# Performance work log

Hardware: AMD Instinct MI355X
Metric: run time of the kernel (lower is better)

## Reference

```python
import jax, jax.numpy as jnp
import numpy as np


def setup_inputs() -> dict:
    key = jax.random.key(0)
    ks = jax.random.split(key, 6)
    B, H, Tq, Tk, D, HID = 2, 4, 512, 512, 64, 128
    return {
        "q": jax.random.normal(ks[0], (B, H, Tq, D), dtype=jnp.float32),
        "k": jax.random.normal(ks[1], (B, H, Tk, D), dtype=jnp.float32),
        # W1 stored math-layout [Dq+Dk, hidden] (torch Linear weight is its transpose)
        "W1": jax.random.normal(ks[2], (2 * D, HID), dtype=jnp.float32) * (1.0 / np.sqrt(2 * D)),
        "b1": jax.random.normal(ks[3], (HID,), dtype=jnp.float32) * 0.02,
        "W2": jax.random.normal(ks[4], (HID, 1), dtype=jnp.float32) * (1.0 / np.sqrt(HID)),
        "b2": jax.random.normal(ks[5], (1,), dtype=jnp.float32) * 0.02,
    }


def reference(q, k, W1, b1, W2, b2):
    """Pairwise MLP scores s[b,h,i,j] = W2 . relu(W1 @ [q_i; k_j] + b1) + b2.

    Linear over cat(q,k) decomposes into separate q/k projections that are
    broadcast-summed, avoiding the [B,H,Tq,Tk,Dq+Dk] concat tensor (same math).
    """
    Dq = q.shape[-1]
    qh = jnp.einsum("bhqd,dc->bhqc", q, W1[:Dq])   # [B,H,Tq,hid]
    kh = jnp.einsum("bhkd,dc->bhkc", k, W1[Dq:])   # [B,H,Tk,hid]
    h = jax.nn.relu(qh[:, :, :, None, :] + kh[:, :, None, :, :] + b1)  # [B,H,Tq,Tk,hid]
    s = jnp.einsum("bhqkc,c->bhqk", h, W2[:, 0]) + b2[0]
    return s
```

## Files before the change

kernel.cpp:

```cpp
#include <hip/hip_runtime.h>

#define T    512
#define D    64
#define HID  128
#define NBH  8
#define NP   (HID / 2)

typedef _Float16 h2 __attribute__((ext_vector_type(2)));

static __device__ __forceinline__ h2 bc_h2(float f) {
    return __builtin_bit_cast(h2, f);
}

__global__ __launch_bounds__(256, 2) void proj_kernel(
    const float* __restrict__ q, const float* __restrict__ k,
    const float* __restrict__ W1, const float* __restrict__ b1,
    h2* __restrict__ qh_h, h2* __restrict__ kh_h)
{
    const int bid    = blockIdx.x;
    const int bh     = bid >> 6;
    const int src    = (bid >> 5) & 1;
    const int chunk  = (bid >> 2) & 7;
    const int csplit = bid & 3;
    const int base_c = csplit * 32;

    const float* __restrict__ X = (src == 0) ? q : k;
    h2* __restrict__ outp       = (src == 0) ? qh_h : kh_h;

    __shared__ float w1t[32][68];

    const int tid = threadIdx.x;
    for (int idx = tid; idx < 32 * 64; idx += 256) {
        const int cc = idx & 31;
        const int d  = idx >> 5;
        w1t[cc][d] = W1[(src * D + d) * HID + base_c + cc];
    }
    __syncthreads();

    const int r  = tid & 63;
    const int cg = tid >> 6;
    const int i  = chunk * 64 + r;

    float xr[D];
    const float4* xrow = (const float4*)(X + (size_t)(bh * T + i) * D);
    #pragma unroll
    for (int t = 0; t < D / 4; ++t) {
        const float4 v = xrow[t];
        xr[4*t+0] = v.x; xr[4*t+1] = v.y; xr[4*t+2] = v.z; xr[4*t+3] = v.w;
    }

    #pragma unroll
    for (int pp = 0; pp < 4; ++pp) {
        const int cc0 = cg * 8 + 2 * pp;
        float acc0 = (src == 0) ? b1[base_c + cc0]     : 0.0f;
        float acc1 = (src == 0) ? b1[base_c + cc0 + 1] : 0.0f;
        const float4* w0 = (const float4*)(&w1t[cc0][0]);
        const float4* w1 = (const float4*)(&w1t[cc0 + 1][0]);
        #pragma unroll
        for (int t = 0; t < D / 4; ++t) {
            const float4 a = w0[t];
            const float4 b = w1[t];
            acc0 += xr[4*t+0]*a.x + xr[4*t+1]*a.y + xr[4*t+2]*a.z + xr[4*t+3]*a.w;
            acc1 += xr[4*t+0]*b.x + xr[4*t+1]*b.y + xr[4*t+2]*b.z + xr[4*t+3]*b.w;
        }
        h2 v;
        v.x = (_Float16)acc0;
        v.y = (_Float16)acc1;
        const int p = csplit * 16 + cg * 4 + pp;
        outp[(size_t)(bh * NP + p) * T + i] = v;
    }
}

__global__ __launch_bounds__(256, 2) void score_kernel(
    const h2* __restrict__ qh_h, const h2* __restrict__ kh_h,
    const float* __restrict__ W2, const float* __restrict__ b2,
    float* __restrict__ out)
{
    const int bid = blockIdx.x;
    const int bh  = bid >> 6;
    const int it  = (bid >> 3) & 7;
    const int jt  = bid & 7;
    const int i0  = it * 64;
    const int j0  = jt * 64;

    __shared__ h2 qt2[NP + 1][64];
    __shared__ h2 kt2[NP + 1][64];
    __shared__ h2 w2h[NP + 4];

    const int tid = threadIdx.x;
    for (int idx = tid; idx < 2 * NP * 16; idx += 256) {
        const int tile = idx >> 10;
        const int p    = (idx >> 4) & 63;
        const int g    = idx & 15;
        const h2* srcp = tile ? kh_h : qh_h;
        const int o0   = tile ? j0 : i0;
        float4 v = ((const float4*)(srcp + (size_t)(bh * NP + p) * T + o0))[g];
        if (tile) ((float4*)&kt2[p][0])[g] = v;
        else      ((float4*)&qt2[p][0])[g] = v;
    }
    if (tid < NP) {
        h2 w;
        w.x = (_Float16)W2[2 * tid];
        w.y = (_Float16)W2[2 * tid + 1];
        w2h[tid] = w;
    }
    __syncthreads();

    const int tx = tid & 15;
    const int ty = tid >> 4;

    const h2* __restrict__ qb = &qt2[0][4 * ty];
    const h2* __restrict__ kb = &kt2[0][4 * tx];

    float acc[4][4];
    #pragma unroll
    for (int m = 0; m < 4; ++m)
        #pragma unroll
        for (int n = 0; n < 4; ++n)
            acc[m][n] = 0.0f;

    const h2 hzero = (h2)(_Float16)0.0f;

    float4 qf = *(const float4*)qb;
    float4 kf = *(const float4*)kb;
    float4 w4 = *(const float4*)&w2h[0];

    for (int pg = 0; pg < 16; ++pg) {
        const float4 w4n = *(const float4*)&w2h[4 * pg + 4];
        #pragma unroll
        for (int s = 0; s < 4; ++s) {
            const int p = 4 * pg + s;
            const float4 qn = *(const float4*)(qb + (size_t)(p + 1) * 64);
            const float4 kn = *(const float4*)(kb + (size_t)(p + 1) * 64);

            const h2 w = bc_h2(s == 0 ? w4.x : s == 1 ? w4.y
                             : s == 2 ? w4.z : w4.w);
            const h2 qv[4] = {bc_h2(qf.x), bc_h2(qf.y), bc_h2(qf.z), bc_h2(qf.w)};
            const h2 kv[4] = {bc_h2(kf.x), bc_h2(kf.y), bc_h2(kf.z), bc_h2(kf.w)};
            #pragma unroll
            for (int m = 0; m < 4; ++m) {
                #pragma unroll
                for (int n = 0; n < 4; ++n) {
                    h2 u = qv[m] + kv[n];
                    u = __builtin_elementwise_max(u, hzero);
                    acc[m][n] = __builtin_amdgcn_fdot2(u, w, acc[m][n], false);
                }
            }
            qf = qn;
            kf = kn;
        }
        w4 = w4n;
    }

    const float bb = b2[0];
    #pragma unroll
    for (int m = 0; m < 4; ++m) {
        const int i = i0 + 4 * ty + m;
        float4 o;
        o.x = acc[m][0] + bb;
        o.y = acc[m][1] + bb;
        o.z = acc[m][2] + bb;
        o.w = acc[m][3] + bb;
        ((float4*)(out + (size_t)(bh * T + i) * T + j0))[tx] = o;
    }
}

extern "C" void kernel_launch(void* const* d_in, const int* in_sizes, int n_in,
                              void* d_out, int out_size, void* d_ws, size_t ws_size,
                              hipStream_t stream) {
    const float* q  = (const float*)d_in[0];
    const float* k  = (const float*)d_in[1];
    const float* W1 = (const float*)d_in[2];
    const float* b1 = (const float*)d_in[3];
    const float* W2 = (const float*)d_in[4];
    const float* b2 = (const float*)d_in[5];
    float* out = (float*)d_out;

    h2* qh_h = (h2*)d_ws;
    h2* kh_h = qh_h + (size_t)NBH * NP * T;

    proj_kernel<<<512, 256, 0, stream>>>(q, k, W1, b1, qh_h, kh_h);
    score_kernel<<<512, 256, 0, stream>>>(qh_h, kh_h, W2, b2, out);
}
```

Baseline: 91.35 us.

## Halve score tile width, double grid, and use inline-asm packed ReLU

The score kernel now uses 64x32 output tiles with a 4x2 micro-tile per thread, launching 1024 blocks instead of 512, with occupancy hint raised to 4 blocks per SM. The explicit register double-buffering of LDS loads is replaced by a simple unrolled loop. The ReLU is now an inline v_pk_max_f16 with an inline constant zero. The goal is more blocks for better CU coverage and latency hiding. The cost is less register reuse per thread, more LDS reads per FMA, and duplicated q-tile loads across blocks.

Result: no change. 92.85 us (+1.6%).

```diff
diff --git a/kernel.cpp b/kernel.cpp
--- a/kernel.cpp
+++ b/kernel.cpp
@@ -10,6 +10,12 @@
 
 static __device__ __forceinline__ h2 bc_h2(float f) {
     return __builtin_bit_cast(h2, f);
+}
+
+static __device__ __forceinline__ h2 relu_h2(h2 x) {
+    h2 r;
+    asm("v_pk_max_f16 %0, %1, 0" : "=v"(r) : "v"(x));
+    return r;
 }
 
 __global__ __launch_bounds__(256, 2) void proj_kernel(
@@ -71,32 +77,36 @@
     }
 }
 
-__global__ __launch_bounds__(256, 2) void score_kernel(
+__global__ __launch_bounds__(256, 4) void score_kernel(
     const h2* __restrict__ qh_h, const h2* __restrict__ kh_h,
     const float* __restrict__ W2, const float* __restrict__ b2,
     float* __restrict__ out)
 {
     const int bid = blockIdx.x;
-    const int bh  = bid >> 6;
-    const int it  = (bid >> 3) & 7;
-    const int jt  = bid & 7;
+    const int bh  = bid >> 7;
+    const int it  = (bid >> 4) & 7;
+    const int jt  = bid & 15;
     const int i0  = it * 64;
-    const int j0  = jt * 64;
+    const int j0  = jt * 32;
 
-    __shared__ h2 qt2[NP + 1][64];
-    __shared__ h2 kt2[NP + 1][64];
-    __shared__ h2 w2h[NP + 4];
+    __shared__ h2 qt2[NP][64];
+    __shared__ h2 kt2[NP][32];
+    __shared__ h2 w2h[NP];
 
     const int tid = threadIdx.x;
-    for (int idx = tid; idx < 2 * NP * 16; idx += 256) {
-        const int tile = idx >> 10;
-        const int p    = (idx >> 4) & 63;
-        const int g    = idx & 15;
-        const h2* srcp = tile ? kh_h : qh_h;
-        const int o0   = tile ? j0 : i0;
-        float4 v = ((const float4*)(srcp + (size_t)(bh * NP + p) * T + o0))[g];
-        if (tile) ((float4*)&kt2[p][0])[g] = v;
-        else      ((float4*)&qt2[p][0])[g] = v;
+    for (int idx = tid; idx < 1536; idx += 256) {
+        if (idx < 1024) {
+            const int p = idx >> 4;
+            const int g = idx & 15;
+            ((float4*)&qt2[p][0])[g] =
+                ((const float4*)(qh_h + (size_t)(bh * NP + p) * T + i0))[g];
+        } else {
+            const int r = idx - 1024;
+            const int p = r >> 3;
+            const int g = r & 7;
+            ((float4*)&kt2[p][0])[g] =
+                ((const float4*)(kh_h + (size_t)(bh * NP + p) * T + j0))[g];
+        }
     }
     if (tid < NP) {
         h2 w;
@@ -109,59 +119,39 @@
     const int tx = tid & 15;
     const int ty = tid >> 4;
 
-    const h2* __restrict__ qb = &qt2[0][4 * ty];
-    const h2* __restrict__ kb = &kt2[0][4 * tx];
+    float acc[4][2];
+    #pragma unroll
+    for (int m = 0; m < 4; ++m) {
+        acc[m][0] = 0.0f;
+        acc[m][1] = 0.0f;
+    }
 
-    float acc[4][4];
-    #pragma unroll
-    for (int m = 0; m < 4; ++m)
+    #pragma unroll 8
+    for (int p = 0; p < NP; ++p) {
+        const float4 qa4 = ((const float4*)&qt2[p][0])[ty];
+        const float2 kb2 = ((const float2*)&kt2[p][0])[tx];
+        const h2 w = w2h[p];
+        const h2 qv[4] = {bc_h2(qa4.x), bc_h2(qa4.y), bc_h2(qa4.z), bc_h2(qa4.w)};
+        const h2 kv[2] = {bc_h2(kb2.x), bc_h2(kb2.y)};
         #pragma unroll
-        for (int n = 0; n < 4; ++n)
-            acc[m][n] = 0.0f;
-
-    const h2 hzero = (h2)(_Float16)0.0f;
-
-    float4 qf = *(const float4*)qb;
-    float4 kf = *(const float4*)kb;
-    float4 w4 = *(const float4*)&w2h[0];
-
-    for (int pg = 0; pg < 16; ++pg) {
-        const float4 w4n = *(const float4*)&w2h[4 * pg + 4];
-        #pragma unroll
-        for (int s = 0; s < 4; ++s) {
-            const int p = 4 * pg + s;
-            const float4 qn = *(const float4*)(qb + (size_t)(p + 1) * 64);
-            const float4 kn = *(const float4*)(kb + (size_t)(p + 1) * 64);
-
-            const h2 w = bc_h2(s == 0 ? w4.x : s == 1 ? w4.y
-                             : s == 2 ? w4.z : w4.w);
-            const h2 qv[4] = {bc_h2(qf.x), bc_h2(qf.y), bc_h2(qf.z), bc_h2(qf.w)};
-            const h2 kv[4] = {bc_h2(kf.x), bc_h2(kf.y), bc_h2(kf.z), bc_h2(kf.w)};
+        for (int m = 0; m < 4; ++m) {
             #pragma unroll
-            for (int m = 0; m < 4; ++m) {
-                #pragma unroll
-                for (int n = 0; n < 4; ++n) {
-                    h2 u = qv[m] + kv[n];
-                    u = __builtin_elementwise_max(u, hzero);
-                    acc[m][n] = __builtin_amdgcn_fdot2(u, w, acc[m][n], false);
-                }
+            for (int n = 0; n < 2; ++n) {
+                h2 u = qv[m] + kv[n];
+                u = relu_h2(u);
+                acc[m][n] = __builtin_amdgcn_fdot2(u, w, acc[m][n], false);
             }
-            qf = qn;
-            kf = kn;
         }
-        w4 = w4n;
     }
 
     const float bb = b2[0];
     #pragma unroll
     for (int m = 0; m < 4; ++m) {
         const int i = i0 + 4 * ty + m;
-        float4 o;
+        float2 o;
         o.x = acc[m][0] + bb;
         o.y = acc[m][1] + bb;
-        o.z = acc[m][2] + bb;
-        o.w = acc[m][3] + bb;
-        ((float4*)(out + (size_t)(bh * T + i) * T + j0))[tx] = o;
+        ((float2*)(out + (size_t)(bh * T + i) * T + j0))[tx] = o;
     }
 }
 
@@ -180,5 +170,5 @@
     h2* kh_h = qh_h + (size_t)NBH * NP * T;
 
     proj_kernel<<<512, 256, 0, stream>>>(q, k, W1, b1, qh_h, kh_h);
-    score_kernel<<<512, 256, 0, stream>>>(qh_h, kh_h, W2, b2, out);
+    score_kernel<<<1024, 256, 0, stream>>>(qh_h, kh_h, W2, b2, out);
 }
```

## Read W1 directly from global in projection, precompute W2 fp16, use inline relu

Applied to the files above, without the earlier changes.

The projection kernel no longer stages a transposed W1 tile in shared memory. Each wave reads eight contiguous W1 columns per d straight from global/cache, using a wave-uniform column index so the loads can be scalar. The fp16 W2 conversion moves into the projection kernel and is written to the workspace, so the score kernel reads it from global memory. The score kernel's hand-pipelined LDS prefetch is replaced by a simple unroll-8 loop, with relu done through inline v_pk_max_f16 asm. This trades the LDS staging and its barrier for more global weight traffic and relies on the compiler to schedule the loop.

Result: slower. 100.6 us (+10.1%).

```diff
diff --git a/kernel.cpp b/kernel.cpp
--- a/kernel.cpp
+++ b/kernel.cpp
@@ -12,34 +12,39 @@
     return __builtin_bit_cast(h2, f);
 }
 
+static __device__ __forceinline__ h2 relu_h2(h2 x) {
+    h2 r;
+    asm("v_pk_max_f16 %0, %1, 0" : "=v"(r) : "v"(x));
+    return r;
+}
+
 __global__ __launch_bounds__(256, 2) void proj_kernel(
     const float* __restrict__ q, const float* __restrict__ k,
     const float* __restrict__ W1, const float* __restrict__ b1,
-    h2* __restrict__ qh_h, h2* __restrict__ kh_h)
+    const float* __restrict__ W2,
+    h2* __restrict__ qh_h, h2* __restrict__ kh_h, h2* __restrict__ w2g)
 {
     const int bid    = blockIdx.x;
     const int bh     = bid >> 6;
     const int src    = (bid >> 5) & 1;
     const int chunk  = (bid >> 2) & 7;
     const int csplit = bid & 3;
-    const int base_c = csplit * 32;
+    const int tid    = threadIdx.x;
+
+    if (bid == 0 && tid < NP) {
+        h2 w;
+        w.x = (_Float16)W2[2 * tid];
+        w.y = (_Float16)W2[2 * tid + 1];
+        w2g[tid] = w;
+    }
+
+    const int r   = tid & 63;
+    const int cgu = __builtin_amdgcn_readfirstlane(tid >> 6);
+    const int c0  = csplit * 32 + cgu * 8;
 
     const float* __restrict__ X = (src == 0) ? q : k;
     h2* __restrict__ outp       = (src == 0) ? qh_h : kh_h;
-
-    __shared__ float w1t[32][68];
-
-    const int tid = threadIdx.x;
-    for (int idx = tid; idx < 32 * 64; idx += 256) {
-        const int cc = idx & 31;
-        const int d  = idx >> 5;
-        w1t[cc][d] = W1[(src * D + d) * HID + base_c + cc];
-    }
-    __syncthreads();
-
-    const int r  = tid & 63;
-    const int cg = tid >> 6;
-    const int i  = chunk * 64 + r;
+    const int i = chunk * 64 + r;
 
     float xr[D];
     const float4* xrow = (const float4*)(X + (size_t)(bh * T + i) * D);
@@ -49,31 +54,36 @@
         xr[4*t+0] = v.x; xr[4*t+1] = v.y; xr[4*t+2] = v.z; xr[4*t+3] = v.w;
     }
 
+    float acc[8];
+    #pragma unroll
+    for (int cc = 0; cc < 8; ++cc)
+        acc[cc] = (src == 0) ? b1[c0 + cc] : 0.0f;
+
+    const float* __restrict__ w1base = W1 + (size_t)src * D * HID + c0;
+    #pragma unroll 8
+    for (int d = 0; d < D; ++d) {
+        const float4 wa = *(const float4*)(w1base + (size_t)d * HID);
+        const float4 wb = *(const float4*)(w1base + (size_t)d * HID + 4);
+        const float x = xr[d];
+        acc[0] += x * wa.x; acc[1] += x * wa.y;
+        acc[2] += x * wa.z; acc[3] += x * wa.w;
+        acc[4] += x * wb.x; acc[5] += x * wb.y;
+        acc[6] += x * wb.z; acc[7] += x * wb.w;
+    }
+
     #pragma unroll
     for (int pp = 0; pp < 4; ++pp) {
-        const int cc0 = cg * 8 + 2 * pp;
-        float acc0 = (src == 0) ? b1[base_c + cc0]     : 0.0f;
-        float acc1 = (src == 0) ? b1[base_c + cc0 + 1] : 0.0f;
-        const float4* w0 = (const float4*)(&w1t[cc0][0]);
-        const float4* w1 = (const float4*)(&w1t[cc0 + 1][0]);
-        #pragma unroll
-        for (int t = 0; t < D / 4; ++t) {
-            const float4 a = w0[t];
-            const float4 b = w1[t];
-            acc0 += xr[4*t+0]*a.x + xr[4*t+1]*a.y + xr[4*t+2]*a.z + xr[4*t+3]*a.w;
-            acc1 += xr[4*t+0]*b.x + xr[4*t+1]*b.y + xr[4*t+2]*b.z + xr[4*t+3]*b.w;
-        }
         h2 v;
-        v.x = (_Float16)acc0;
-        v.y = (_Float16)acc1;
-        const int p = csplit * 16 + cg * 4 + pp;
+        v.x = (_Float16)acc[2 * pp];
+        v.y = (_Float16)acc[2 * pp + 1];
+        const int p = (c0 >> 1) + pp;
         outp[(size_t)(bh * NP + p) * T + i] = v;
     }
 }
 
 __global__ __launch_bounds__(256, 2) void score_kernel(
     const h2* __restrict__ qh_h, const h2* __restrict__ kh_h,
-    const float* __restrict__ W2, const float* __restrict__ b2,
+    const h2* __restrict__ w2g, const float* __restrict__ b2,
     float* __restrict__ out)
 {
     const int bid = blockIdx.x;
@@ -83,9 +93,8 @@
     const int i0  = it * 64;
     const int j0  = jt * 64;
 
-    __shared__ h2 qt2[NP + 1][64];
-    __shared__ h2 kt2[NP + 1][64];
-    __shared__ h2 w2h[NP + 4];
+    __shared__ h2 qt2[NP][64];
+    __shared__ h2 kt2[NP][64];
 
     const int tid = threadIdx.x;
     for (int idx = tid; idx < 2 * NP * 16; idx += 256) {
@@ -98,19 +107,10 @@
         if (tile) ((float4*)&kt2[p][0])[g] = v;
         else      ((float4*)&qt2[p][0])[g] = v;
     }
-    if (tid < NP) {
-        h2 w;
-        w.x = (_Float16)W2[2 * tid];
-        w.y = (_Float16)W2[2 * tid + 1];
-        w2h[tid] = w;
-    }
     __syncthreads();
 
     const int tx = tid & 15;
     const int ty = tid >> 4;
-
-    const h2* __restrict__ qb = &qt2[0][4 * ty];
-    const h2* __restrict__ kb = &kt2[0][4 * tx];
 
     float acc[4][4];
     #pragma unroll
@@ -119,37 +119,22 @@
         for (int n = 0; n < 4; ++n)
             acc[m][n] = 0.0f;
 
-    const h2 hzero = (h2)(_Float16)0.0f;
-
-    float4 qf = *(const float4*)qb;
-    float4 kf = *(const float4*)kb;
-    float4 w4 = *(const float4*)&w2h[0];
-
-    for (int pg = 0; pg < 16; ++pg) {
-        const float4 w4n = *(const float4*)&w2h[4 * pg + 4];
+    #pragma unroll 8
+    for (int p = 0; p < NP; ++p) {
+        const h2 w = w2g[p];
+        const float4 qa4 = ((const float4*)&qt2[p][0])[ty];
+        const float4 kb4 = ((const float4*)&kt2[p][0])[tx];
+        const h2 qv[4] = {bc_h2(qa4.x), bc_h2(qa4.y), bc_h2(qa4.z), bc_h2(qa4.w)};
+        const h2 kv[4] = {bc_h2(kb4.x), bc_h2(kb4.y), bc_h2(kb4.z), bc_h2(kb4.w)};
         #pragma unroll
-        for (int s = 0; s < 4; ++s) {
-            const int p = 4 * pg + s;
-            const float4 qn = *(const float4*)(qb + (size_t)(p + 1) * 64);
-            const float4 kn = *(const float4*)(kb + (size_t)(p + 1) * 64);
-
-            const h2 w = bc_h2(s == 0 ? w4.x : s == 1 ? w4.y
-                             : s == 2 ? w4.z : w4.w);
-            const h2 qv[4] = {bc_h2(qf.x), bc_h2(qf.y), bc_h2(qf.z), bc_h2(qf.w)};
-            const h2 kv[4] = {bc_h2(kf.x), bc_h2(kf.y), bc_h2(kf.z), bc_h2(kf.w)};
+        for (int m = 0; m < 4; ++m) {
             #pragma unroll
-            for (int m = 0; m < 4; ++m) {
-                #pragma unroll
-                for (int n = 0; n < 4; ++n) {
-                    h2 u = qv[m] + kv[n];
-                    u = __builtin_elementwise_max(u, hzero);
-                    acc[m][n] = __builtin_amdgcn_fdot2(u, w, acc[m][n], false);
-                }
+            for (int n = 0; n < 4; ++n) {
+                h2 u = qv[m] + kv[n];
+                u = relu_h2(u);
+                acc[m][n] = __builtin_amdgcn_fdot2(u, w, acc[m][n], false);
             }
-            qf = qn;
-            kf = kn;
         }
-        w4 = w4n;
     }
 
     const float bb = b2[0];
@@ -178,7 +163,8 @@
 
     h2* qh_h = (h2*)d_ws;
     h2* kh_h = qh_h + (size_t)NBH * NP * T;
+    h2* w2g  = kh_h + (size_t)NBH * NP * T;
 
-    proj_kernel<<<512, 256, 0, stream>>>(q, k, W1, b1, qh_h, kh_h);
-    score_kernel<<<512, 256, 0, stream>>>(qh_h, kh_h, W2, b2, out);
+    proj_kernel<<<512, 256, 0, stream>>>(q, k, W1, b1, W2, qh_h, kh_h, w2g);
+    score_kernel<<<512, 256, 0, stream>>>(qh_h, kh_h, w2g, b2, out);
 }
```
